# Optimization experiments

Hardware: AMD Instinct MI355X
Metric: run time of the kernel (lower is better)

## Reference

```python
import jax, jax.numpy as jnp
import numpy as np

B, K, D = 8, 2048, 1024

def setup_inputs() -> dict:
    key = jax.random.key(0)
    k1, k2 = jax.random.split(key)
    x = jax.random.normal(k1, (B, K, D), dtype=jnp.float32)
    W = jax.random.normal(k2, (K, K), dtype=jnp.float32) * 0.02  # dt_proj weight [out=K, in=K]
    b = jnp.zeros((K,), dtype=jnp.float32)                        # dt_proj bias
    return {"x": x, "W": W, "b": b}

def _scan_combine(c1, c2):
    # compose affine maps s -> a*s + u; (a1,u1) then (a2,u2)
    a1, u1 = c1
    a2, u2 = c2
    return (a2 * a1, a2 * u1 + u2)

def reference(x, W, b):
    # lam[b,t,d] = sigmoid( sum_k x[b,k,d] * W[t,k] + b[t] )
    # (dt_proj is a Linear over the TIME axis after permute(0,2,1))
    lam = jax.nn.sigmoid(jnp.einsum('bkd,tk->btd', x, W) + b[None, :, None])
    # s_t = lam_t * s_{t-1} + (1 - lam_t) * x_t, s_0 = 0  -> associative scan over time
    _, ys = jax.lax.associative_scan(_scan_combine, (lam, (1.0 - lam) * x), axis=1)
    return ys
```

## Files before the change

kernel.cpp:

```cpp
#include <hip/hip_runtime.h>
#include <hip/hip_bf16.h>
#include <stdint.h>

#define B_ 8
#define K_ 2048
#define D_ 1024
#define NC 32
#define TC (K_ / NC)

typedef float v4f __attribute__((ext_vector_type(4)));
typedef short v8s __attribute__((ext_vector_type(8)));

__device__ __forceinline__ unsigned short f2bf(float f) {
    __hip_bfloat16 h = __float2bfloat16(f);
    return *reinterpret_cast<unsigned short*>(&h);
}

__device__ __forceinline__ void async_ld16(const void* g, void* l) {
    __builtin_amdgcn_global_load_lds(
        (__attribute__((address_space(1))) void*)(void*)g,
        (__attribute__((address_space(3))) void*)l,
        16, 0, 0);
}

__global__ void conv_w(const float* __restrict__ W, unsigned short* __restrict__ Wb) {
    int i = (blockIdx.x * 256 + threadIdx.x) * 4;
    float4 v = *(const float4*)(W + i);
    ushort4 o;
    o.x = f2bf(v.x); o.y = f2bf(v.y); o.z = f2bf(v.z); o.w = f2bf(v.w);
    *(ushort4*)(Wb + i) = o;
}

__global__ void conv_x_t(const float* __restrict__ x, unsigned short* __restrict__ xT) {
    const int k0 = blockIdx.x * 64, d0 = blockIdx.y * 64, bb = blockIdx.z;
    __shared__ unsigned short tile[64][68];
    const int tid = threadIdx.x;
    const int tx = tid & 15, ty = tid >> 4;
    const float* xp = x + (size_t)bb * K_ * D_;
#pragma unroll
    for (int r = 0; r < 4; r++) {
        int row = ty + r * 16;
        float4 v = *(const float4*)(xp + (size_t)(k0 + row) * D_ + d0 + tx * 4);
        tile[row][tx * 4 + 0] = f2bf(v.x);
        tile[row][tx * 4 + 1] = f2bf(v.y);
        tile[row][tx * 4 + 2] = f2bf(v.z);
        tile[row][tx * 4 + 3] = f2bf(v.w);
    }
    __syncthreads();
    unsigned short* op = xT + (size_t)bb * D_ * K_;
#pragma unroll
    for (int r = 0; r < 4; r++) {
        int dcol = ty + r * 16;
        ushort4 u;
        u.x = tile[tx * 4 + 0][dcol];
        u.y = tile[tx * 4 + 1][dcol];
        u.z = tile[tx * 4 + 2][dcol];
        u.w = tile[tx * 4 + 3][dcol];
        *(ushort4*)(op + (size_t)(d0 + dcol) * K_ + k0 + tx * 4) = u;
    }
}

__launch_bounds__(512, 2)
__global__ void gemm_sig(const unsigned short* __restrict__ Wb,
                         const unsigned short* __restrict__ xT,
                         const float* __restrict__ bias,
                         float* __restrict__ lam) {
    __shared__ unsigned short As[2][2][256 * 32];
    __shared__ unsigned short Bs[2][2][256 * 32];

    const int bid = blockIdx.x;
    const int lid = (bid & 7) * 32 + (bid >> 3);
    const int bb = lid >> 5;
    const int tM = (lid >> 2) & 7;
    const int tN = lid & 3;

    const int tid = threadIdx.x;
    const int w = tid >> 6;
    const int lane = tid & 63;
    const int wm = w >> 2;
    const int wn = w & 3;
    const int quad = lane >> 4;
    const int l16 = lane & 15;

    const unsigned short* Ag = Wb + (size_t)(tM * 256) * K_;
    const unsigned short* Bg = xT + (size_t)bb * D_ * K_ + (size_t)(tN * 256) * K_;

    const int srow = lane >> 2;
    const int sgk8 = ((lane & 3) ^ ((lane >> 3) & 3)) * 8;

    const int frg = (quad ^ ((l16 >> 1) & 3)) * 8;
    const int aoff = (wm * 128 + l16) * 32 + frg;
    const int boff = (wn * 64 + l16) * 32 + frg;

    v4f acc[8][4];
#pragma unroll
    for (int i = 0; i < 8; i++)
#pragma unroll
        for (int j = 0; j < 4; j++) acc[i][j] = (v4f)0.f;

#define STAGE_(dst, bufi, kh, kk, Gp)                                                   \
    do {                                                                                \
        async_ld16(Gp + (size_t)(w * 16 + srow) * K_ + (kk) + (kh) * 32 + sgk8,         \
                   &dst[bufi][kh][w * 512]);                                            \
        async_ld16(Gp + (size_t)((8 + w) * 16 + srow) * K_ + (kk) + (kh) * 32 + sgk8,   \
                   &dst[bufi][kh][(8 + w) * 512]);                                      \
    } while (0)

    STAGE_(As, 0, 0, 0, Ag);
    STAGE_(Bs, 0, 0, 0, Bg);
    STAGE_(As, 0, 1, 0, Ag);
    STAGE_(Bs, 0, 1, 0, Bg);
    asm volatile("s_waitcnt vmcnt(4)");
    asm volatile("s_barrier" ::: "memory");

    v8s af[8], bf[2];

    for (int t = 0; t < K_ / 64; ++t) {
        const int cur = t & 1, nxt = cur ^ 1;
        int k1 = (t + 1) * 64;
        if (k1 == K_) k1 = 0;

#pragma unroll
        for (int i = 0; i < 8; i++) af[i] = *(const v8s*)(&As[cur][0][aoff + i * 512]);
        bf[0] = *(const v8s*)(&Bs[cur][0][boff]);
        bf[1] = *(const v8s*)(&Bs[cur][0][boff + 512]);
        STAGE_(As, nxt, 0, k1, Ag);
        asm volatile("s_barrier" ::: "memory");
        asm volatile("s_waitcnt lgkmcnt(0)");
        __builtin_amdgcn_s_setprio(1);
#pragma unroll
        for (int i = 0; i < 8; i++) {
            acc[i][0] = __builtin_amdgcn_mfma_f32_16x16x32_bf16(af[i], bf[0], acc[i][0], 0, 0, 0);
            acc[i][1] = __builtin_amdgcn_mfma_f32_16x16x32_bf16(af[i], bf[1], acc[i][1], 0, 0, 0);
        }
        __builtin_amdgcn_s_setprio(0);
        asm volatile("s_barrier" ::: "memory");

        bf[0] = *(const v8s*)(&Bs[cur][0][boff + 2 * 512]);
        bf[1] = *(const v8s*)(&Bs[cur][0][boff + 3 * 512]);
        STAGE_(Bs, nxt, 0, k1, Bg);
        asm volatile("s_barrier" ::: "memory");
        asm volatile("s_waitcnt lgkmcnt(0)");
        __builtin_amdgcn_s_setprio(1);
#pragma unroll
        for (int i = 0; i < 8; i++) {
            acc[i][2] = __builtin_amdgcn_mfma_f32_16x16x32_bf16(af[i], bf[0], acc[i][2], 0, 0, 0);
            acc[i][3] = __builtin_amdgcn_mfma_f32_16x16x32_bf16(af[i], bf[1], acc[i][3], 0, 0, 0);
        }
        __builtin_amdgcn_s_setprio(0);
        asm volatile("s_waitcnt vmcnt(4)");
        asm volatile("s_barrier" ::: "memory");

#pragma unroll
        for (int i = 0; i < 8; i++) af[i] = *(const v8s*)(&As[cur][1][aoff + i * 512]);
        bf[0] = *(const v8s*)(&Bs[cur][1][boff]);
        bf[1] = *(const v8s*)(&Bs[cur][1][boff + 512]);
        STAGE_(As, nxt, 1, k1, Ag);
        asm volatile("s_barrier" ::: "memory");
        asm volatile("s_waitcnt lgkmcnt(0)");
        __builtin_amdgcn_s_setprio(1);
#pragma unroll
        for (int i = 0; i < 8; i++) {
            acc[i][0] = __builtin_amdgcn_mfma_f32_16x16x32_bf16(af[i], bf[0], acc[i][0], 0, 0, 0);
            acc[i][1] = __builtin_amdgcn_mfma_f32_16x16x32_bf16(af[i], bf[1], acc[i][1], 0, 0, 0);
        }
        __builtin_amdgcn_s_setprio(0);
        asm volatile("s_barrier" ::: "memory");

        bf[0] = *(const v8s*)(&Bs[cur][1][boff + 2 * 512]);
        bf[1] = *(const v8s*)(&Bs[cur][1][boff + 3 * 512]);
        STAGE_(Bs, nxt, 1, k1, Bg);
        asm volatile("s_barrier" ::: "memory");
        asm volatile("s_waitcnt lgkmcnt(0)");
        __builtin_amdgcn_s_setprio(1);
#pragma unroll
        for (int i = 0; i < 8; i++) {
            acc[i][2] = __builtin_amdgcn_mfma_f32_16x16x32_bf16(af[i], bf[0], acc[i][2], 0, 0, 0);
            acc[i][3] = __builtin_amdgcn_mfma_f32_16x16x32_bf16(af[i], bf[1], acc[i][3], 0, 0, 0);
        }
        __builtin_amdgcn_s_setprio(0);
        asm volatile("s_waitcnt vmcnt(4)");
        asm volatile("s_barrier" ::: "memory");
    }
#undef STAGE_

    float* out = lam + (size_t)bb * K_ * D_;
#pragma unroll
    for (int i = 0; i < 8; i++) {
        int rowb = tM * 256 + wm * 128 + i * 16 + quad * 4;
#pragma unroll
        for (int r = 0; r < 4; r++) {
            float bt = bias[rowb + r];
#pragma unroll
            for (int j = 0; j < 4; j++) {
                int col = tN * 256 + wn * 64 + j * 16 + l16;
                float v = acc[i][j][r] + bt;
                out[(size_t)(rowb + r) * D_ + col] = 1.f / (1.f + __expf(-v));
            }
        }
    }
}

__global__ void scan_pass1(const float* __restrict__ lam, const float* __restrict__ x,
                           float* __restrict__ Ac, float* __restrict__ Uc) {
    int id = blockIdx.x * 256 + threadIdx.x;
    int d2 = (id & 511) * 2;
    int c = (id >> 9) & (NC - 1);
    int bb = id >> 14;
    const float* lp = lam + ((size_t)bb * K_ + (size_t)c * TC) * D_ + d2;
    const float* xp = x   + ((size_t)bb * K_ + (size_t)c * TC) * D_ + d2;
    float2 A = make_float2(1.f, 1.f), U = make_float2(0.f, 0.f);
#pragma unroll 8
    for (int t = 0; t < TC; t++) {
        float2 l  = *(const float2*)(lp + (size_t)t * D_);
        float2 xv = *(const float2*)(xp + (size_t)t * D_);
        A.x *= l.x; A.y *= l.y;
        U.x = l.x * U.x + (1.f - l.x) * xv.x;
        U.y = l.y * U.y + (1.f - l.y) * xv.y;
    }
    size_t oi = ((size_t)bb * NC + c) * D_ + d2;
    *(float2*)(Ac + oi) = A;
    *(float2*)(Uc + oi) = U;
}

__global__ void scan_pass2(const float* __restrict__ Ac, const float* __restrict__ Uc,
                           float* __restrict__ Sin) {
    int id = blockIdx.x * 256 + threadIdx.x;
    int d = id & (D_ - 1);
    int bb = id >> 10;
    float s = 0.f;
#pragma unroll
    for (int c = 0; c < NC; c++) {
        int idx = (bb * NC + c) * D_ + d;
        Sin[idx] = s;
        s = Ac[idx] * s + Uc[idx];
    }
}

__global__ void scan_pass3(const float* __restrict__ x, const float* __restrict__ Sin,
                           float* __restrict__ lamout) {
    int id = blockIdx.x * 256 + threadIdx.x;
    int d2 = (id & 511) * 2;
    int c = (id >> 9) & (NC - 1);
    int bb = id >> 14;
    float* lp = lamout + ((size_t)bb * K_ + (size_t)c * TC) * D_ + d2;
    const float* xp = x + ((size_t)bb * K_ + (size_t)c * TC) * D_ + d2;
    size_t si = ((size_t)bb * NC + c) * D_ + d2;
    float2 s = *(const float2*)(Sin + si);
#pragma unroll 8
    for (int t = 0; t < TC; t++) {
        float2 l  = *(const float2*)(lp + (size_t)t * D_);
        float2 xv = *(const float2*)(xp + (size_t)t * D_);
        s.x = l.x * s.x + (1.f - l.x) * xv.x;
        s.y = l.y * s.y + (1.f - l.y) * xv.y;
        *(float2*)(lp + (size_t)t * D_) = s;
    }
}

extern "C" void kernel_launch(void* const* d_in, const int* in_sizes, int n_in,
                              void* d_out, int out_size, void* d_ws, size_t ws_size,
                              hipStream_t stream) {
    const float* x    = (const float*)d_in[0];
    const float* W    = (const float*)d_in[1];
    const float* bias = (const float*)d_in[2];
    float* out = (float*)d_out;
    char* ws = (char*)d_ws;

    unsigned short* xT = (unsigned short*)ws;
    unsigned short* Wb = (unsigned short*)(ws + 33554432);
    float* Ac  = (float*)(ws + 33554432);
    float* Uc  = (float*)(ws + 33554432 + 1048576);
    float* Sin = (float*)(ws + 33554432 + 2097152);

    conv_w<<<dim3(K_ * K_ / 4 / 256), 256, 0, stream>>>(W, Wb);
    conv_x_t<<<dim3(K_ / 64, D_ / 64, B_), 256, 0, stream>>>(x, xT);
    gemm_sig<<<dim3(256), dim3(512), 0, stream>>>(Wb, xT, bias, out);
    scan_pass1<<<dim3(B_ * NC * D_ / 2 / 256), 256, 0, stream>>>(out, x, Ac, Uc);
    scan_pass2<<<dim3(B_ * D_ / 256), 256, 0, stream>>>(Ac, Uc, Sin);
    scan_pass3<<<dim3(B_ * NC * D_ / 2 / 256), 256, 0, stream>>>(x, Sin, out);
}
```

Baseline: 244.2 us.

## Fuse per-chunk scan reduction into GEMM epilogue via LDS staging

The GEMM epilogue now writes each wave's sigmoid tile into swizzled LDS and computes the per-chunk scan aggregates (A, U) directly. This removes the separate scan_pass1 kernel and its re-read of lam from global memory. The fused path is taken only when the workspace is large enough, and it adds serial per-lane scan work to the GEMM tail. scan_pass2 is also relaunched with 64-thread blocks to spread its work across more blocks, and sched_barriers are added around the MFMA phases.

```diff
diff --git a/kernel.cpp b/kernel.cpp
--- a/kernel.cpp
+++ b/kernel.cpp
@@ -64,9 +64,12 @@
 __global__ void gemm_sig(const unsigned short* __restrict__ Wb,
                          const unsigned short* __restrict__ xT,
                          const float* __restrict__ bias,
-                         float* __restrict__ lam) {
-    __shared__ unsigned short As[2][2][256 * 32];
-    __shared__ unsigned short Bs[2][2][256 * 32];
+                         const float* __restrict__ xf,
+                         float* __restrict__ lam,
+                         float* __restrict__ Ac,
+                         float* __restrict__ Uc,
+                         int fuse) {
+    __shared__ __align__(16) unsigned short smem_all[2][2][2][256 * 32];
 
     const int bid = blockIdx.x;
     const int lid = (bid & 7) * 32 + (bid >> 3);
@@ -98,18 +101,18 @@
 #pragma unroll
         for (int j = 0; j < 4; j++) acc[i][j] = (v4f)0.f;
 
-#define STAGE_(dst, bufi, kh, kk, Gp)                                                   \
-    do {                                                                                \
-        async_ld16(Gp + (size_t)(w * 16 + srow) * K_ + (kk) + (kh) * 32 + sgk8,         \
-                   &dst[bufi][kh][w * 512]);                                            \
-        async_ld16(Gp + (size_t)((8 + w) * 16 + srow) * K_ + (kk) + (kh) * 32 + sgk8,   \
-                   &dst[bufi][kh][(8 + w) * 512]);                                      \
+#define STAGE_(op, bufi, kh, kk, Gp)                                                        \
+    do {                                                                                    \
+        async_ld16(Gp + (size_t)(w * 16 + srow) * K_ + (kk) + (kh) * 32 + sgk8,             \
+                   &smem_all[op][bufi][kh][w * 512]);                                       \
+        async_ld16(Gp + (size_t)((8 + w) * 16 + srow) * K_ + (kk) + (kh) * 32 + sgk8,       \
+                   &smem_all[op][bufi][kh][(8 + w) * 512]);                                 \
     } while (0)
 
-    STAGE_(As, 0, 0, 0, Ag);
-    STAGE_(Bs, 0, 0, 0, Bg);
-    STAGE_(As, 0, 1, 0, Ag);
-    STAGE_(Bs, 0, 1, 0, Bg);
+    STAGE_(0, 0, 0, 0, Ag);
+    STAGE_(1, 0, 0, 0, Bg);
+    STAGE_(0, 0, 1, 0, Ag);
+    STAGE_(1, 0, 1, 0, Bg);
     asm volatile("s_waitcnt vmcnt(4)");
     asm volatile("s_barrier" ::: "memory");
 
@@ -121,12 +124,13 @@
         if (k1 == K_) k1 = 0;
 
 #pragma unroll
-        for (int i = 0; i < 8; i++) af[i] = *(const v8s*)(&As[cur][0][aoff + i * 512]);
-        bf[0] = *(const v8s*)(&Bs[cur][0][boff]);
-        bf[1] = *(const v8s*)(&Bs[cur][0][boff + 512]);
-        STAGE_(As, nxt, 0, k1, Ag);
+        for (int i = 0; i < 8; i++) af[i] = *(const v8s*)(&smem_all[0][cur][0][aoff + i * 512]);
+        bf[0] = *(const v8s*)(&smem_all[1][cur][0][boff]);
+        bf[1] = *(const v8s*)(&smem_all[1][cur][0][boff + 512]);
+        STAGE_(0, nxt, 0, k1, Ag);
         asm volatile("s_barrier" ::: "memory");
         asm volatile("s_waitcnt lgkmcnt(0)");
+        __builtin_amdgcn_sched_barrier(0);
         __builtin_amdgcn_s_setprio(1);
 #pragma unroll
         for (int i = 0; i < 8; i++) {
@@ -136,11 +140,12 @@
         __builtin_amdgcn_s_setprio(0);
         asm volatile("s_barrier" ::: "memory");
 
-        bf[0] = *(const v8s*)(&Bs[cur][0][boff + 2 * 512]);
-        bf[1] = *(const v8s*)(&Bs[cur][0][boff + 3 * 512]);
-        STAGE_(Bs, nxt, 0, k1, Bg);
+        bf[0] = *(const v8s*)(&smem_all[1][cur][0][boff + 2 * 512]);
+        bf[1] = *(const v8s*)(&smem_all[1][cur][0][boff + 3 * 512]);
+        STAGE_(1, nxt, 0, k1, Bg);
         asm volatile("s_barrier" ::: "memory");
         asm volatile("s_waitcnt lgkmcnt(0)");
+        __builtin_amdgcn_sched_barrier(0);
         __builtin_amdgcn_s_setprio(1);
 #pragma unroll
         for (int i = 0; i < 8; i++) {
@@ -152,12 +157,13 @@
         asm volatile("s_barrier" ::: "memory");
 
 #pragma unroll
-        for (int i = 0; i < 8; i++) af[i] = *(const v8s*)(&As[cur][1][aoff + i * 512]);
-        bf[0] = *(const v8s*)(&Bs[cur][1][boff]);
-        bf[1] = *(const v8s*)(&Bs[cur][1][boff + 512]);
-        STAGE_(As, nxt, 1, k1, Ag);
+        for (int i = 0; i < 8; i++) af[i] = *(const v8s*)(&smem_all[0][cur][1][aoff + i * 512]);
+        bf[0] = *(const v8s*)(&smem_all[1][cur][1][boff]);
+        bf[1] = *(const v8s*)(&smem_all[1][cur][1][boff + 512]);
+        STAGE_(0, nxt, 1, k1, Ag);
         asm volatile("s_barrier" ::: "memory");
         asm volatile("s_waitcnt lgkmcnt(0)");
+        __builtin_amdgcn_sched_barrier(0);
         __builtin_amdgcn_s_setprio(1);
 #pragma unroll
         for (int i = 0; i < 8; i++) {
@@ -167,11 +173,12 @@
         __builtin_amdgcn_s_setprio(0);
         asm volatile("s_barrier" ::: "memory");
 
-        bf[0] = *(const v8s*)(&Bs[cur][1][boff + 2 * 512]);
-        bf[1] = *(const v8s*)(&Bs[cur][1][boff + 3 * 512]);
-        STAGE_(Bs, nxt, 1, k1, Bg);
+        bf[0] = *(const v8s*)(&smem_all[1][cur][1][boff + 2 * 512]);
+        bf[1] = *(const v8s*)(&smem_all[1][cur][1][boff + 3 * 512]);
+        STAGE_(1, nxt, 1, k1, Bg);
         asm volatile("s_barrier" ::: "memory");
         asm volatile("s_waitcnt lgkmcnt(0)");
+        __builtin_amdgcn_sched_barrier(0);
         __builtin_amdgcn_s_setprio(1);
 #pragma unroll
         for (int i = 0; i < 8; i++) {
@@ -184,18 +191,66 @@
     }
 #undef STAGE_
 
+    asm volatile("s_waitcnt vmcnt(0)");
+    asm volatile("s_barrier" ::: "memory");
+
     float* out = lam + (size_t)bb * K_ * D_;
-#pragma unroll
-    for (int i = 0; i < 8; i++) {
-        int rowb = tM * 256 + wm * 128 + i * 16 + quad * 4;
-#pragma unroll
-        for (int r = 0; r < 4; r++) {
-            float bt = bias[rowb + r];
-#pragma unroll
-            for (int j = 0; j < 4; j++) {
-                int col = tN * 256 + wn * 64 + j * 16 + l16;
-                float v = acc[i][j][r] + bt;
-                out[(size_t)(rowb + r) * D_ + col] = 1.f / (1.f + __expf(-v));
+    const int dg = tN * 256 + wn * 64;
+
+    if (fuse) {
+        float* Swp = (float*)smem_all + w * 4096;
+        const int swzw = quad * 16;
+#pragma unroll
+        for (int cg = 0; cg < 2; cg++) {
+            const int c = tM * 4 + wm * 2 + cg;
+            const int t0 = c * 64;
+#pragma unroll
+            for (int ii = 0; ii < 4; ii++) {
+                int i = cg * 4 + ii;
+                int rowb = t0 + ii * 16 + quad * 4;
+                int Rb = ii * 16 + quad * 4;
+#pragma unroll
+                for (int r = 0; r < 4; r++) {
+                    float bt = bias[rowb + r];
+#pragma unroll
+                    for (int j = 0; j < 4; j++) {
+                        int colc = j * 16 + l16;
+                        float v = acc[i][j][r] + bt;
+                        float sg = 1.f / (1.f + __expf(-v));
+                        out[(size_t)(rowb + r) * D_ + dg + colc] = sg;
+                        Swp[(Rb + r) * 64 + (colc ^ swzw)] = sg;
+                    }
+                }
+            }
+            asm volatile("s_waitcnt lgkmcnt(0)");
+            __builtin_amdgcn_sched_barrier(0);
+            const float* xg = xf + ((size_t)bb * K_ + t0) * D_ + dg + lane;
+            float A = 1.f, U = 0.f;
+#pragma unroll 8
+            for (int tt = 0; tt < 64; tt++) {
+                float l = Swp[tt * 64 + (lane ^ (((tt >> 2) & 3) * 16))];
+                float xv = xg[(size_t)tt * D_];
+                A *= l;
+                U = l * U + (1.f - l) * xv;
+            }
+            size_t oi = ((size_t)bb * NC + c) * D_ + dg + lane;
+            Ac[oi] = A;
+            Uc[oi] = U;
+            __builtin_amdgcn_sched_barrier(0);
+        }
+    } else {
+#pragma unroll
+        for (int i = 0; i < 8; i++) {
+            int rowb = tM * 256 + wm * 128 + i * 16 + quad * 4;
+#pragma unroll
+            for (int r = 0; r < 4; r++) {
+                float bt = bias[rowb + r];
+#pragma unroll
+                for (int j = 0; j < 4; j++) {
+                    int col = tN * 256 + wn * 64 + j * 16 + l16;
+                    float v = acc[i][j][r] + bt;
+                    out[(size_t)(rowb + r) * D_ + col] = 1.f / (1.f + __expf(-v));
+                }
             }
         }
     }
@@ -225,7 +280,7 @@
 
 __global__ void scan_pass2(const float* __restrict__ Ac, const float* __restrict__ Uc,
                            float* __restrict__ Sin) {
-    int id = blockIdx.x * 256 + threadIdx.x;
+    int id = blockIdx.x * 64 + threadIdx.x;
     int d = id & (D_ - 1);
     int bb = id >> 10;
     float s = 0.f;
@@ -268,14 +323,23 @@
 
     unsigned short* xT = (unsigned short*)ws;
     unsigned short* Wb = (unsigned short*)(ws + 33554432);
-    float* Ac  = (float*)(ws + 33554432);
-    float* Uc  = (float*)(ws + 33554432 + 1048576);
+
+    const int fuse = (ws_size >= 44040192u) ? 1 : 0;
+    float* Ac, * Uc;
+    if (fuse) {
+        Ac = (float*)(ws + 41943040);
+        Uc = (float*)(ws + 41943040 + 1048576);
+    } else {
+        Ac = (float*)(ws + 33554432);
+        Uc = (float*)(ws + 33554432 + 1048576);
+    }
     float* Sin = (float*)(ws + 33554432 + 2097152);
 
     conv_w<<<dim3(K_ * K_ / 4 / 256), 256, 0, stream>>>(W, Wb);
     conv_x_t<<<dim3(K_ / 64, D_ / 64, B_), 256, 0, stream>>>(x, xT);
-    gemm_sig<<<dim3(256), dim3(512), 0, stream>>>(Wb, xT, bias, out);
-    scan_pass1<<<dim3(B_ * NC * D_ / 2 / 256), 256, 0, stream>>>(out, x, Ac, Uc);
-    scan_pass2<<<dim3(B_ * D_ / 256), 256, 0, stream>>>(Ac, Uc, Sin);
+    gemm_sig<<<dim3(256), dim3(512), 0, stream>>>(Wb, xT, bias, x, out, Ac, Uc, fuse);
+    if (!fuse)
+        scan_pass1<<<dim3(B_ * NC * D_ / 2 / 256), 256, 0, stream>>>(out, x, Ac, Uc);
+    scan_pass2<<<dim3(B_ * D_ / 64), 64, 0, stream>>>(Ac, Uc, Sin);
     scan_pass3<<<dim3(B_ * NC * D_ / 2 / 256), 256, 0, stream>>>(x, Sin, out);
 }
```

Result: faster. 237.5 us (-2.8%).
